# Performance work log

Hardware: AMD Instinct MI355X
Metric: run time of the kernel (lower is better)

The kernel has to match this reference:

```python
import jax, jax.numpy as jnp
import numpy as np

HEAD_DIM = 128
NUM_HEADS = 16
GROUP_SIZE = 8


def setup_inputs() -> dict:
    key = jax.random.key(0)
    k1, k2, k3 = jax.random.split(key, 3)
    B, T, K = 2, 2048, 2048
    query = jax.random.normal(k1, (B, T, NUM_HEADS * HEAD_DIM), dtype=jnp.float32)
    k_ = jax.random.normal(k2, (B, K, NUM_HEADS, HEAD_DIM), dtype=jnp.float32)
    v_ = jax.random.normal(k3, (B, K, NUM_HEADS, HEAD_DIM), dtype=jnp.float32)
    return {"query": query, "key": k_, "value": v_}


def reference(query, key, value):
    B, T, _ = query.shape
    g = GROUP_SIZE
    # (B, T//g, g, H, D)
    gq = query.reshape(B, T // g, g, NUM_HEADS, HEAD_DIM)
    scale = jnp.sqrt(jnp.asarray(HEAD_DIM, dtype=query.dtype))
    # scores: (B, T//g, g, H, K)
    scores = jnp.einsum('btghd,bkhd->btghk', gq, key) / scale
    attention = jax.nn.softmax(scores, axis=-1)
    out = jnp.einsum('btghk,bkhd->btghd', attention, value)
    return out.reshape(B, T, -1)
```

## Files before the change

kernel.cpp:

```cpp
#include <hip/hip_runtime.h>


#define T_   2048
#define KLEN 2048
#define H_   16
#define D_   128
#define BH_  32
#define NT_  (KLEN / 64)

typedef unsigned short u16;
typedef short bf16x8 __attribute__((ext_vector_type(8), may_alias));
typedef float f32x4 __attribute__((ext_vector_type(4)));
typedef float f32x8 __attribute__((ext_vector_type(8), may_alias));
typedef float f32x16 __attribute__((ext_vector_type(16)));
typedef unsigned int u32a __attribute__((may_alias));
typedef u16 u16a __attribute__((may_alias));

__device__ __forceinline__ u16 f2bf(float f) {
    unsigned int u = __builtin_bit_cast(unsigned int, f);
    u += 0x7fffu + ((u >> 16) & 1u);
    return (u16)(u >> 16);
}
__device__ __forceinline__ unsigned int pk2(float a, float b) {
    unsigned int r;
    asm("v_cvt_pk_bf16_f32 %0, %1, %2" : "=v"(r) : "v"(a), "v"(b));
    return r;
}
__device__ __forceinline__ void pl_swap(unsigned int& a, unsigned int& b) {
    asm("v_permlane32_swap_b32 %0, %1" : "+v"(a), "+v"(b));
}

__device__ __forceinline__ void async_cp16(const void* g, void* l) {
    __builtin_amdgcn_global_load_lds(
        (const __attribute__((address_space(1))) unsigned int*)g,
        (__attribute__((address_space(3))) unsigned int*)l, 16, 0, 0);
}

#define FR_ELEMS ((size_t)KLEN * D_)
#define WS_NEED  (2 * BH_ * FR_ELEMS * sizeof(u16))
#define SM_BUF   32768

__global__ __launch_bounds__(256)
void prep_fused(const float* __restrict__ k_g, const float* __restrict__ v_g,
                u16* __restrict__ kf, u16* __restrict__ vf) {
    __shared__ __align__(16) unsigned char smk[16384];
    __shared__ __align__(16) unsigned char smv[16384];
    const int kt64 = blockIdx.x & 31;
    const int bh   = blockIdx.x >> 5;
    const int b = bh >> 4, h = bh & 15;
    const int tid = threadIdx.x;

    {
        const float* kbase = k_g + ((size_t)(b * KLEN + kt64 * 64) * H_ + h) * D_;
        #pragma unroll
        for (int i = 0; i < 4; ++i) {
            const int gid  = tid + 256 * i;
            const int row  = gid >> 4;
            const int col8 = gid & 15;
            f32x8 kv = *(const f32x8*)(kbase + (size_t)row * (H_ * D_) + col8 * 8);
            uint4 w;
            w.x = pk2(kv[0], kv[1]); w.y = pk2(kv[2], kv[3]);
            w.z = pk2(kv[4], kv[5]); w.w = pk2(kv[6], kv[7]);
            *(uint4*)(smk + row * 256 + ((col8 ^ (row & 15)) * 16)) = w;
        }
    }
    {
        const float* vbase = v_g + ((size_t)b * KLEN * H_ + h) * D_;
        const int sc0 = tid & 15;
        const int spr = tid >> 4;
        #pragma unroll
        for (int rr = 0; rr < 2; ++rr) {
            const int r0 = 2 * (spr + 16 * rr);
            const float* vp = vbase + (size_t)(kt64 * 64 + r0) * (H_ * D_) + sc0 * 8;
            f32x8 va = *(const f32x8*)vp;
            f32x8 vb = *(const f32x8*)(vp + H_ * D_);
            const int g_hi = r0 >> 3;
            const int woff = (r0 & 7) * 2;
            #pragma unroll
            for (int j = 0; j < 8; ++j) {
                const int d = sc0 * 8 + j;
                const int g = g_hi ^ ((d ^ (d >> 3)) & 7);
                *(u32a*)(smv + d * 128 + g * 16 + woff) = pk2(va[j], vb[j]);
            }
        }
    }
    __syncthreads();
    {
        u16* obase = kf + (size_t)bh * FR_ELEMS + (size_t)kt64 * 8192;
        #pragma unroll
        for (int i = 0; i < 4; ++i) {
            const int gid    = tid + 256 * i;
            const int lane   = gid & 63;
            const int dchunk = (gid >> 6) & 7;
            const int ktile  = gid >> 9;
            const int key  = ktile * 32 + (lane & 31);
            const int col8 = dchunk * 2 + (lane >> 5);
            uint4 w = *(const uint4*)(smk + key * 256 + ((col8 ^ (key & 15)) * 16));
            *(uint4*)(obase + (size_t)gid * 8) = w;
        }
    }
    {
        u16* obase = vf + (size_t)bh * FR_ELEMS;
        #pragma unroll
        for (int i = 0; i < 4; ++i) {
            const int gid   = tid + 256 * i;
            const int lane  = gid & 63;
            const int ntile = (gid >> 6) & 3;
            const int kc    = (gid >> 8) & 3;
            const int key0  = kc * 16 + (lane >> 5) * 8;
            const int d     = ntile * 32 + (lane & 31);
            const int g     = (key0 >> 3) ^ ((d ^ (d >> 3)) & 7);
            uint4 w = *(const uint4*)(smv + d * 128 + g * 16);
            *(uint4*)(obase + ((size_t)(kt64 * 16 + kc * 4 + ntile) * 64 + lane) * 8) = w;
        }
    }
}


struct PA2 { bf16x8 f0, f1; };

__device__ __forceinline__ PA2 softmax_pack(f32x16 st, float kexp, float& lacc) {
    float p[16];
    #pragma unroll
    for (int r = 0; r < 16; ++r) p[r] = exp2f(st[r] * kexp);
    lacc += (((p[0] + p[1]) + (p[2] + p[3])) + ((p[4] + p[5]) + (p[6] + p[7])))
          + (((p[8] + p[9]) + (p[10] + p[11])) + ((p[12] + p[13]) + (p[14] + p[15])));
    unsigned int a0 = pk2(p[0], p[1]),   b0 = pk2(p[4], p[5]);
    unsigned int a1 = pk2(p[2], p[3]),   b1 = pk2(p[6], p[7]);
    unsigned int a2 = pk2(p[8], p[9]),   b2 = pk2(p[12], p[13]);
    unsigned int a3 = pk2(p[10], p[11]), b3 = pk2(p[14], p[15]);
    pl_swap(a0, b0); pl_swap(a1, b1); pl_swap(a2, b2); pl_swap(a3, b3);
    uint4 w0; w0.x = a0; w0.y = a1; w0.z = b0; w0.w = b1;
    uint4 w1; w1.x = a2; w1.y = a3; w1.z = b2; w1.w = b3;
    PA2 r;
    r.f0 = __builtin_bit_cast(bf16x8, w0);
    r.f1 = __builtin_bit_cast(bf16x8, w1);
    return r;
}

__global__ __launch_bounds__(512, 2)
void gqa_fa5(const float* __restrict__ q_g, const u16* __restrict__ kf,
             const u16* __restrict__ vf, float* __restrict__ o_g) {
    __shared__ __align__(16) unsigned char smem[2 * SM_BUF];

    const int lane = threadIdx.x & 63;
    const int wave = threadIdx.x >> 6;
    const int half = lane >> 5;
    const int col  = lane & 31;

    const int blk = blockIdx.x;
    const int bh  = (blk & 7) * 4 + (blk >> 6);
    const int qt  = (blk >> 3) & 7;
    const int b = bh >> 4, h = bh & 15;

    const int q0 = qt * 256 + wave * 32;

    bf16x8 qf[8];
    {
        const float* qbase = q_g + (size_t)(b * T_ + q0 + col) * (H_ * D_)
                                 + h * D_ + half * 8;
        #pragma unroll
        for (int dchunk = 0; dchunk < 8; ++dchunk) {
            f32x8 qv = *(const f32x8*)(qbase + dchunk * 16);
            uint4 w;
            w.x = pk2(qv[0], qv[1]); w.y = pk2(qv[2], qv[3]);
            w.z = pk2(qv[4], qv[5]); w.w = pk2(qv[6], qv[7]);
            qf[dchunk] = __builtin_bit_cast(bf16x8, w);
        }
    }

    const u16* KFb = kf + (size_t)bh * FR_ELEMS;
    const u16* VFb = vf + (size_t)bh * FR_ELEMS;

    f32x16 acc[4] = {};
    float l_part = 0.f;

    const float kexp = 0.12751744f;

    auto stage = [&](int buf, int kt) {
        const u16* ksrc = KFb + (size_t)kt * 8192;
        const u16* vsrc = VFb + (size_t)kt * 8192;
        unsigned char* base = smem + buf * SM_BUF;
        #pragma unroll
        for (int j = 0; j < 4; ++j) {
            const int idx = wave * 4 + j;
            if (idx < 16)
                async_cp16(ksrc + idx * 512 + lane * 8, base + idx * 1024);
            else
                async_cp16(vsrc + (idx - 16) * 512 + lane * 8,
                           base + 16384 + (idx - 16) * 1024);
        }
    };

    stage(0, 0);
    __syncthreads();

    for (int kt = 0; kt < NT_; ++kt) {
        const int cur = kt & 1;
        if (kt + 1 < NT_) stage(cur ^ 1, kt + 1);

        const unsigned char* kbuf = smem + cur * SM_BUF;
        const unsigned char* vbuf = kbuf + 16384;

        f32x16 s0 = {}, s1 = {};
        __builtin_amdgcn_s_setprio(1);
        #pragma unroll
        for (int dchunk = 0; dchunk < 8; ++dchunk) {
            bf16x8 kfr0 = *(const bf16x8*)(kbuf + dchunk * 1024 + lane * 16);
            bf16x8 kfr1 = *(const bf16x8*)(kbuf + (8 + dchunk) * 1024 + lane * 16);
            s0 = __builtin_amdgcn_mfma_f32_32x32x16_bf16(kfr0, qf[dchunk], s0, 0, 0, 0);
            s1 = __builtin_amdgcn_mfma_f32_32x32x16_bf16(kfr1, qf[dchunk], s1, 0, 0, 0);
        }
        __builtin_amdgcn_s_setprio(0);

        PA2 pa01 = softmax_pack(s0, kexp, l_part);
        PA2 pa23 = softmax_pack(s1, kexp, l_part);

        bf16x8 pfrag0 = pa01.f0, pfrag1 = pa01.f1;
        bf16x8 pfrag2 = pa23.f0, pfrag3 = pa23.f1;
        __builtin_amdgcn_s_setprio(1);
        #pragma unroll
        for (int kc = 0; kc < 4; ++kc) {
            const bf16x8 paf = (kc == 0) ? pfrag0 : (kc == 1) ? pfrag1
                             : (kc == 2) ? pfrag2 : pfrag3;
            #pragma unroll
            for (int nt2 = 0; nt2 < 4; ++nt2) {
                bf16x8 vfr = *(const bf16x8*)(vbuf + (kc * 4 + nt2) * 1024 + lane * 16);
                acc[nt2] = __builtin_amdgcn_mfma_f32_32x32x16_bf16(paf, vfr, acc[nt2], 0, 0, 0);
            }
        }
        __builtin_amdgcn_s_setprio(0);

        __syncthreads();
    }

    const float l_full = l_part + __shfl_xor(l_part, 32);
    float* lds_l = (float*)smem;
    if (half == 0) lds_l[wave * 32 + col] = 1.f / l_full;
    __syncthreads();
    #pragma unroll
    for (int r = 0; r < 16; ++r) {
        const int qrow = (r & 3) + 8 * (r >> 2) + 4 * half;
        const float inv = lds_l[wave * 32 + qrow];
        float* op = o_g + (size_t)(b * T_ + q0 + qrow) * (H_ * D_) + h * D_ + col;
        #pragma unroll
        for (int nt2 = 0; nt2 < 4; ++nt2)
            op[nt2 * 32] = acc[nt2][r] * inv;
    }
}


#define VT_BYTES 16384
#define KT_BYTES (64 * 136 * 2)
#define PWF_BYTES 2304

__global__ __launch_bounds__(256, 2)
void gqa_fa_v1(const float* __restrict__ q_g, const float* __restrict__ k_g,
               const float* __restrict__ v_g, float* __restrict__ o_g) {
    __shared__ __align__(16) unsigned char smem[VT_BYTES + KT_BYTES + 4 * PWF_BYTES];
    unsigned char* VtB = smem;
    unsigned char* KtB = smem + VT_BYTES;
    const int lane = threadIdx.x & 63;
    const int wave = threadIdx.x >> 6;
    const int c    = lane & 15;
    const int quad = lane >> 4;
    const int qt = blockIdx.x & 31;
    const int bh = blockIdx.x >> 5;
    const int h  = bh & 15;
    const int b  = bh >> 4;
    const int q0 = qt * 64 + wave * 16;
    bf16x8 qf[4];
    {
        const float* qbase = q_g + (size_t)(b * T_ + q0 + c) * (H_ * D_) + h * D_ + quad * 8;
        #pragma unroll
        for (int dc = 0; dc < 4; ++dc) {
            f32x8 qv = *(const f32x8*)(qbase + dc * 32);
            uint4 w;
            w.x = pk2(qv[0], qv[1]); w.y = pk2(qv[2], qv[3]);
            w.z = pk2(qv[4], qv[5]); w.w = pk2(qv[6], qv[7]);
            qf[dc] = __builtin_bit_cast(bf16x8, w);
        }
    }
    f32x4 acc_o[8];
    #pragma unroll
    for (int dt = 0; dt < 8; ++dt) acc_o[dt] = (f32x4){0.f, 0.f, 0.f, 0.f};
    float m_i[4], l_i[4];
    #pragma unroll
    for (int r = 0; r < 4; ++r) { m_i[r] = -1e30f; l_i[r] = 0.f; }
    const float kexp = 0.12751744f;
    unsigned char* Pw = smem + VT_BYTES + KT_BYTES + wave * PWF_BYTES;
    const int sc0 = threadIdx.x & 15;
    const int spr = threadIdx.x >> 4;
    const size_t kvstride = (size_t)(H_ * D_);
    const float* kbase = k_g + ((size_t)b * KLEN * H_ + h) * D_;
    const float* vbase = v_g + ((size_t)b * KLEN * H_ + h) * D_;
    for (int kt = 0; kt < KLEN / 64; ++kt) {
        __syncthreads();
        #pragma unroll
        for (int i = 0; i < 4; ++i) {
            const int id   = threadIdx.x + 256 * i;
            const int row  = id >> 4;
            const int dcol = (id & 15) * 8;
            const float* kp = kbase + (size_t)(kt * 64 + row) * kvstride + dcol;
            f32x8 kv = *(const f32x8*)kp;
            uint4 w;
            w.x = pk2(kv[0], kv[1]); w.y = pk2(kv[2], kv[3]);
            w.z = pk2(kv[4], kv[5]); w.w = pk2(kv[6], kv[7]);
            *(uint4*)(KtB + (row * 136 + dcol) * 2) = w;
        }
        #pragma unroll
        for (int rr = 0; rr < 2; ++rr) {
            const int r0 = 2 * (spr + 16 * rr);
            const float* vp = vbase + (size_t)(kt * 64 + r0) * kvstride + sc0 * 8;
            f32x8 va = *(const f32x8*)vp;
            f32x8 vb = *(const f32x8*)(vp + kvstride);
            const int g_hi = r0 >> 3;
            const int woff = (r0 & 7) * 2;
            #pragma unroll
            for (int j = 0; j < 8; ++j) {
                const int d = sc0 * 8 + j;
                const int g = g_hi ^ ((d ^ (d >> 3)) & 7);
                *(u32a*)(VtB + d * 128 + g * 16 + woff) = pk2(va[j], vb[j]);
            }
        }
        __syncthreads();
        f32x4 s[4];
        #pragma unroll
        for (int nt = 0; nt < 4; ++nt) {
            s[nt] = (f32x4){0.f, 0.f, 0.f, 0.f};
            const u16* kfp = (const u16*)KtB + (nt * 16 + c) * 136 + quad * 8;
            #pragma unroll
            for (int dc = 0; dc < 4; ++dc) {
                bf16x8 kfr = *(const bf16x8*)(kfp + dc * 32);
                s[nt] = __builtin_amdgcn_mfma_f32_16x16x32_bf16(qf[dc], kfr, s[nt], 0, 0, 0);
            }
        }
        #pragma unroll
        for (int r = 0; r < 4; ++r) {
            float v = fmaxf(fmaxf(s[0][r], s[1][r]), fmaxf(s[2][r], s[3][r]));
            v = fmaxf(v, __shfl_xor(v, 1));
            v = fmaxf(v, __shfl_xor(v, 2));
            v = fmaxf(v, __shfl_xor(v, 4));
            v = fmaxf(v, __shfl_xor(v, 8));
            const float mnew  = fmaxf(m_i[r], v);
            const float alpha = exp2f((m_i[r] - mnew) * kexp);
            m_i[r] = mnew;
            l_i[r] *= alpha;
            #pragma unroll
            for (int dt = 0; dt < 8; ++dt) acc_o[dt][r] *= alpha;
            float sum = 0.f;
            #pragma unroll
            for (int nt = 0; nt < 4; ++nt) {
                const float p = exp2f((s[nt][r] - mnew) * kexp);
                sum += p;
                *(u16a*)(Pw + ((quad * 4 + r) * 72 + nt * 16 + c) * 2) = f2bf(p);
            }
            float t = sum;
            t += __shfl_xor(t, 1);
            t += __shfl_xor(t, 2);
            t += __shfl_xor(t, 4);
            t += __shfl_xor(t, 8);
            l_i[r] += t;
        }
        __syncthreads();
        #pragma unroll
        for (int kc = 0; kc < 2; ++kc) {
            bf16x8 pf = *(const bf16x8*)(Pw + (c * 72 + kc * 32 + quad * 8) * 2);
            const int k0 = kc * 32 + quad * 8;
            #pragma unroll
            for (int dt = 0; dt < 8; ++dt) {
                const int d = dt * 16 + c;
                const int g = (k0 >> 3) ^ ((d ^ (d >> 3)) & 7);
                bf16x8 vfr = *(const bf16x8*)(VtB + d * 128 + g * 16);
                acc_o[dt] = __builtin_amdgcn_mfma_f32_16x16x32_bf16(pf, vfr, acc_o[dt], 0, 0, 0);
            }
        }
    }
    #pragma unroll
    for (int r = 0; r < 4; ++r) {
        const float inv = 1.f / l_i[r];
        const int qrow = q0 + quad * 4 + r;
        float* op = o_g + (size_t)(b * T_ + qrow) * (H_ * D_) + h * D_ + c;
        #pragma unroll
        for (int dt = 0; dt < 8; ++dt)
            op[dt * 16] = acc_o[dt][r] * inv;
    }
}

extern "C" void kernel_launch(void* const* d_in, const int* in_sizes, int n_in,
                              void* d_out, int out_size, void* d_ws, size_t ws_size,
                              hipStream_t stream) {
    const float* q = (const float*)d_in[0];
    const float* k = (const float*)d_in[1];
    const float* v = (const float*)d_in[2];
    float* o = (float*)d_out;
    if (ws_size >= WS_NEED) {
        u16* kfb = (u16*)d_ws;
        u16* vfb = kfb + (size_t)BH_ * FR_ELEMS;
        prep_fused<<<dim3(1024), dim3(256), 0, stream>>>(k, v, kfb, vfb);
        gqa_fa5<<<dim3(256), dim3(512), 0, stream>>>(q, kfb, vfb, o);
    } else {
        gqa_fa_v1<<<dim3(1024), dim3(256), 0, stream>>>(q, k, v, o);
    }
}
```

Measured before the change: 206.0 us.

## Software-pipeline QK of next tile with softmax/PV of previous tile, triple-buffer LDS

Restructures the main loop so the QK^T MFMA for tile kt runs before the softmax and PV of tile kt-1, letting the exp/pack VALU work overlap with matrix ops. LDS grows from two to three K/V buffers so the previous tile's V stays resident while the next tile is prefetched. This costs more registers for the carried score accumulators and more shared memory, which may reduce occupancy under launch_bounds(512,2).

```diff
diff --git a/kernel.cpp b/kernel.cpp
--- a/kernel.cpp
+++ b/kernel.cpp
@@ -139,9 +139,9 @@
 }
 
 __global__ __launch_bounds__(512, 2)
-void gqa_fa5(const float* __restrict__ q_g, const u16* __restrict__ kf,
+void gqa_fa8(const float* __restrict__ q_g, const u16* __restrict__ kf,
              const u16* __restrict__ vf, float* __restrict__ o_g) {
-    __shared__ __align__(16) unsigned char smem[2 * SM_BUF];
+    __shared__ __align__(16) unsigned char smem[3 * SM_BUF];
 
     const int lane = threadIdx.x & 63;
     const int wave = threadIdx.x >> 6;
@@ -192,37 +192,26 @@
         }
     };
 
-    stage(0, 0);
-    __syncthreads();
-
-    for (int kt = 0; kt < NT_; ++kt) {
-        const int cur = kt & 1;
-        if (kt + 1 < NT_) stage(cur ^ 1, kt + 1);
-
-        const unsigned char* kbuf = smem + cur * SM_BUF;
-        const unsigned char* vbuf = kbuf + 16384;
-
-        f32x16 s0 = {}, s1 = {};
+    auto qk_tile = [&](const unsigned char* kbuf, f32x16& d0, f32x16& d1) {
         __builtin_amdgcn_s_setprio(1);
         #pragma unroll
         for (int dchunk = 0; dchunk < 8; ++dchunk) {
             bf16x8 kfr0 = *(const bf16x8*)(kbuf + dchunk * 1024 + lane * 16);
             bf16x8 kfr1 = *(const bf16x8*)(kbuf + (8 + dchunk) * 1024 + lane * 16);
-            s0 = __builtin_amdgcn_mfma_f32_32x32x16_bf16(kfr0, qf[dchunk], s0, 0, 0, 0);
-            s1 = __builtin_amdgcn_mfma_f32_32x32x16_bf16(kfr1, qf[dchunk], s1, 0, 0, 0);
+            d0 = __builtin_amdgcn_mfma_f32_32x32x16_bf16(kfr0, qf[dchunk], d0, 0, 0, 0);
+            d1 = __builtin_amdgcn_mfma_f32_32x32x16_bf16(kfr1, qf[dchunk], d1, 0, 0, 0);
         }
         __builtin_amdgcn_s_setprio(0);
-
-        PA2 pa01 = softmax_pack(s0, kexp, l_part);
-        PA2 pa23 = softmax_pack(s1, kexp, l_part);
-
-        bf16x8 pfrag0 = pa01.f0, pfrag1 = pa01.f1;
-        bf16x8 pfrag2 = pa23.f0, pfrag3 = pa23.f1;
+    };
+
+    auto sm_pv = [&](f32x16 t0, f32x16 t1, const unsigned char* vbuf) {
+        PA2 pa01 = softmax_pack(t0, kexp, l_part);
+        PA2 pa23 = softmax_pack(t1, kexp, l_part);
         __builtin_amdgcn_s_setprio(1);
         #pragma unroll
         for (int kc = 0; kc < 4; ++kc) {
-            const bf16x8 paf = (kc == 0) ? pfrag0 : (kc == 1) ? pfrag1
-                             : (kc == 2) ? pfrag2 : pfrag3;
+            const bf16x8 paf = (kc == 0) ? pa01.f0 : (kc == 1) ? pa01.f1
+                             : (kc == 2) ? pa23.f0 : pa23.f1;
             #pragma unroll
             for (int nt2 = 0; nt2 < 4; ++nt2) {
                 bf16x8 vfr = *(const bf16x8*)(vbuf + (kc * 4 + nt2) * 1024 + lane * 16);
@@ -230,9 +219,29 @@
             }
         }
         __builtin_amdgcn_s_setprio(0);
-
+    };
+
+    stage(0, 0);
+    __syncthreads();
+    stage(1, 1);
+    f32x16 ps0 = {}, ps1 = {};
+    qk_tile(smem, ps0, ps1);
+    __syncthreads();
+
+    int cur = 1, prev = 0;
+    for (int kt = 1; kt < NT_; ++kt) {
+        const int nxt = (cur == 2) ? 0 : cur + 1;
+        if (kt + 1 < NT_) stage(nxt, kt + 1);
+
+        f32x16 ns0 = {}, ns1 = {};
+        qk_tile(smem + cur * SM_BUF, ns0, ns1);
+        sm_pv(ps0, ps1, smem + prev * SM_BUF + 16384);
+
+        ps0 = ns0; ps1 = ns1;
+        prev = cur; cur = nxt;
         __syncthreads();
     }
+    sm_pv(ps0, ps1, smem + prev * SM_BUF + 16384);
 
     const float l_full = l_part + __shfl_xor(l_part, 32);
     float* lds_l = (float*)smem;
@@ -398,7 +407,7 @@
         u16* kfb = (u16*)d_ws;
         u16* vfb = kfb + (size_t)BH_ * FR_ELEMS;
         prep_fused<<<dim3(1024), dim3(256), 0, stream>>>(k, v, kfb, vfb);
-        gqa_fa5<<<dim3(256), dim3(512), 0, stream>>>(q, kfb, vfb, o);
+        gqa_fa8<<<dim3(256), dim3(512), 0, stream>>>(q, kfb, vfb, o);
     } else {
         gqa_fa_v1<<<dim3(1024), dim3(256), 0, stream>>>(q, k, v, o);
     }
```

Result: no change. 204.8 us (-0.6%).
